# Performance work log

Measured on AMD Instinct MI355X. Metric: run time of the kernel, lower is better.

Reference implementation:

```python
import jax, jax.numpy as jnp
import numpy as np

NUM_HEADS = 4

def setup_inputs() -> dict:
    key = jax.random.key(0)
    k1, k2, k3, k4 = jax.random.split(key, 4)
    B, N, D = 8, 768, 2048
    x = jax.random.normal(k1, (B, N, D), dtype=jnp.float32)
    s = 1.0 / np.sqrt(N)
    W_qk = jax.random.normal(k2, (N, N), dtype=jnp.float32) * s
    W_v = jax.random.normal(k3, (N, N), dtype=jnp.float32) * s
    W_out = jax.random.normal(k4, (N, N), dtype=jnp.float32) * s
    return {"x": x, "W_qk": W_qk, "W_v": W_v, "W_out": W_out}

def reference(x, W_qk, W_v, W_out):
    B, N, D = x.shape
    H = NUM_HEADS
    n = N // H
    y = jnp.swapaxes(x, 1, 2)                    # (B, D, N): attention over channels D
    qk = y @ W_qk.T                              # (B, D, N)
    v = y @ W_v.T                                # (B, D, N)
    # to heads: (B, D, N) -> (B, H, D, n)
    qk = jnp.swapaxes(qk.reshape(B, D, H, n), 1, 2)
    v = jnp.swapaxes(v.reshape(B, D, H, n), 1, 2)
    dot = jnp.einsum('bhdn,bhen->bhde', qk, qk)  # (B, H, D, D)
    q2 = jnp.sum(qk * qk, axis=-1)               # (B, H, D)
    # negative squared Euclidean distance logits: 2*q.k - ||q||^2 - ||k||^2
    logits = 2.0 * dot - q2[..., :, None] - q2[..., None, :]
    attn = jax.nn.softmax(logits, axis=-1)
    w = jnp.einsum('bhde,bhen->bhdn', attn, v)   # (B, H, D, n)
    # from heads: (B, H, D, n) -> (B, D, N)
    w = jnp.swapaxes(w, 1, 2).reshape(B, D, N)
    out = w @ W_out.T                            # (B, D, N)
    return jnp.swapaxes(out, 1, 2)               # (B, N, D)
```

## Files before the change

### kernel.cpp

```cpp
#include <hip/hip_runtime.h>
#include <stdint.h>

#define B_  8
#define N_  768
#define D_  2048
#define H_  4
#define HN  192

#define QROW 200
#define VROW 72
#define KTILE_B 25600
#define VTILE_B 27648

typedef unsigned short u16;
typedef float    f32x4 __attribute__((ext_vector_type(4)));
typedef __bf16   bf16x8 __attribute__((ext_vector_type(8)));
typedef uint32_t u32x4 __attribute__((ext_vector_type(4)));
typedef uint32_t u32x2 __attribute__((ext_vector_type(2)));

__device__ __forceinline__ u16 f2bf(float f) {
  uint32_t u = __builtin_bit_cast(uint32_t, f);
  u += 0x7fffu + ((u >> 16) & 1u);
  return (u16)(u >> 16);
}

typedef const __attribute__((address_space(1))) void* gas_ptr;
typedef __attribute__((address_space(3))) void* las_ptr;
__device__ __forceinline__ void gld16(const void* g, void* l) {
  __builtin_amdgcn_global_load_lds((gas_ptr)g, (las_ptr)l, 16, 0, 0);
}

__global__ __launch_bounds__(256) void transpose_x(const float* __restrict__ x,
                                                   u16* __restrict__ xt) {
  __shared__ float tile[64][65];
  const int d0 = blockIdx.x * 64;
  const int n0 = blockIdx.y * 64;
  const int b  = blockIdx.z;
  const int t   = threadIdx.x;
  const int col = t & 63;
  const int rb  = (t >> 6) * 16;
  const float* src = x + ((size_t)b * N_ + n0) * D_ + d0;
  #pragma unroll
  for (int i = 0; i < 16; i++)
    tile[rb + i][col] = src[(size_t)(rb + i) * D_ + col];
  __syncthreads();
  u16* dst = xt + ((size_t)b * D_ + d0) * N_ + n0;
  #pragma unroll
  for (int i = 0; i < 16; i++)
    dst[(size_t)(rb + i) * N_ + col] = f2bf(tile[col][rb + i]);
}

__global__ __launch_bounds__(256) void cvt_w(const float* __restrict__ a,
                                             const float* __restrict__ b,
                                             const float* __restrict__ c,
                                             u16* __restrict__ oa,
                                             u16* __restrict__ ob,
                                             u16* __restrict__ oc) {
  const float* src = (blockIdx.y == 0) ? a : ((blockIdx.y == 1) ? b : c);
  u16*         dst = (blockIdx.y == 0) ? oa : ((blockIdx.y == 1) ? ob : oc);
  const int i = (blockIdx.x * 256 + threadIdx.x) * 4;
  f32x4 v = *(const f32x4*)(src + i);
  u16 tmp[4];
  #pragma unroll
  for (int j = 0; j < 4; j++) tmp[j] = f2bf(v[j]);
  *(u32x2*)(dst + i) = *(u32x2*)tmp;
}

__global__ __launch_bounds__(256) void zero_q2(float* __restrict__ q2) {
  q2[blockIdx.x * 256 + threadIdx.x] = 0.f;
}

__global__ __launch_bounds__(256) void qkv_gemm(const u16* __restrict__ xt,
                                                const u16* __restrict__ wqk,
                                                const u16* __restrict__ wv,
                                                u16* __restrict__ qkb,
                                                u16* __restrict__ vtb,
                                                float* __restrict__ q2) {
  const int b  = blockIdx.z;
  const int dtile = blockIdx.x;
  const int d0 = dtile * 64;
  const int j0 = blockIdx.y * 64;
  const int h   = j0 / HN;
  const int jn0 = j0 - h * HN;
  const int tid  = threadIdx.x;
  const int wave = tid >> 6, lane = tid & 63;
  const int l15  = lane & 15, quad = lane >> 4;
  const int wm = wave >> 1, wn = wave & 1;

  __shared__ u16 At[64][40];
  __shared__ u16 Bq[64][40];
  __shared__ u16 Bv[64][40];
  __shared__ float ttile[64][76];

  const f32x4 fz = {0.f, 0.f, 0.f, 0.f};
  f32x4 accq[2][2], accv[2][2];
  #pragma unroll
  for (int i = 0; i < 2; i++)
    #pragma unroll
    for (int j = 0; j < 2; j++) { accq[i][j] = fz; accv[i][j] = fz; }

  const int srow = tid >> 2;
  const int soff = (tid & 3) * 8;
  const u16* ax = xt  + ((size_t)b * D_ + d0 + srow) * N_ + soff;
  const u16* bq = wqk + (size_t)(j0 + srow) * N_ + soff;
  const u16* bv = wv  + (size_t)(j0 + srow) * N_ + soff;

  for (int k0 = 0; k0 < N_; k0 += 32) {
    __syncthreads();
    *(u32x4*)&At[srow][soff] = *(const u32x4*)(ax + k0);
    *(u32x4*)&Bq[srow][soff] = *(const u32x4*)(bq + k0);
    *(u32x4*)&Bv[srow][soff] = *(const u32x4*)(bv + k0);
    __syncthreads();
    bf16x8 Af[2], Bqf[2], Bvf[2];
    #pragma unroll
    for (int mi = 0; mi < 2; mi++)
      Af[mi] = *(const bf16x8*)&At[wm * 32 + mi * 16 + l15][quad * 8];
    #pragma unroll
    for (int ni = 0; ni < 2; ni++) {
      Bqf[ni] = *(const bf16x8*)&Bq[wn * 32 + ni * 16 + l15][quad * 8];
      Bvf[ni] = *(const bf16x8*)&Bv[wn * 32 + ni * 16 + l15][quad * 8];
    }
    #pragma unroll
    for (int mi = 0; mi < 2; mi++)
      #pragma unroll
      for (int ni = 0; ni < 2; ni++) {
        accq[mi][ni] = __builtin_amdgcn_mfma_f32_16x16x32_bf16(Af[mi], Bqf[ni], accq[mi][ni], 0, 0, 0);
        accv[mi][ni] = __builtin_amdgcn_mfma_f32_16x16x32_bf16(Af[mi], Bvf[ni], accv[mi][ni], 0, 0, 0);
      }
  }

  const size_t bh = (size_t)(b * H_ + h);

  #pragma unroll
  for (int mi = 0; mi < 2; mi++)
    #pragma unroll
    for (int r = 0; r < 4; r++) {
      const int d = d0 + wm * 32 + mi * 16 + quad * 4 + r;
      float ssq = 0.f;
      #pragma unroll
      for (int ni = 0; ni < 2; ni++) {
        float val = accq[mi][ni][r];
        ssq += val * val;
      }
      ssq += __shfl_xor(ssq, 1, 64);
      ssq += __shfl_xor(ssq, 2, 64);
      ssq += __shfl_xor(ssq, 4, 64);
      ssq += __shfl_xor(ssq, 8, 64);
      if (l15 == 0) atomicAdd(&q2[bh * D_ + d], ssq);
    }

  #pragma unroll
  for (int mi = 0; mi < 2; mi++)
    #pragma unroll
    for (int ni = 0; ni < 2; ni++)
      #pragma unroll
      for (int r = 0; r < 4; r++)
        ttile[wm * 32 + mi * 16 + quad * 4 + r][wn * 32 + ni * 16 + l15] = accq[mi][ni][r];
  __syncthreads();
  u16* qtbase = qkb + bh * (size_t)(D_ * QROW);
  #pragma unroll
  for (int i = 0; i < 2; i++) {
    const int p = tid + i * 256;
    const int d = p & 63, g8 = p >> 6;
    u16 tmp[8];
    #pragma unroll
    for (int j = 0; j < 8; j++) tmp[j] = f2bf(ttile[d][g8 * 8 + j]);
    *(u32x4*)(qtbase + (size_t)(d0 + d) * QROW + jn0 + g8 * 8) = *(u32x4*)tmp;
  }
  __syncthreads();

  #pragma unroll
  for (int mi = 0; mi < 2; mi++)
    #pragma unroll
    for (int ni = 0; ni < 2; ni++)
      *(f32x4*)&ttile[wn * 32 + ni * 16 + l15][wm * 32 + mi * 16 + quad * 4] = accv[mi][ni];
  __syncthreads();
  u16* vtbase = vtb + bh * (size_t)(32 * HN * VROW) + (size_t)dtile * (HN * VROW);
  #pragma unroll
  for (int i = 0; i < 2; i++) {
    const int p = tid + i * 256;
    const int jn = p & 63, e8 = p >> 6;
    u16 tmp[8];
    #pragma unroll
    for (int j = 0; j < 8; j++) tmp[j] = f2bf(ttile[jn][e8 * 8 + j]);
    *(u32x4*)(vtbase + (size_t)(jn0 + jn) * VROW + e8 * 8) = *(u32x4*)tmp;
  }
}

__global__ __launch_bounds__(256, 2) void attn_kernel(const u16* __restrict__ qkb,
                                                      const u16* __restrict__ vtb,
                                                      const float* __restrict__ q2,
                                                      u16* __restrict__ wbuf) {
  const int bid  = blockIdx.x;
  const int bh   = (bid & 7) * 4 + (bid >> 7);
  const int dblk = (bid >> 3) & 15;
  const int b = bh >> 2, h = bh & 3;
  const int tid  = threadIdx.x;
  const int wave = tid >> 6, lane = tid & 63;
  const int l15  = lane & 15, quad = lane >> 4;

  __shared__ u16 Klds[64 * QROW];
  __shared__ u16 Vlds[HN * VROW];
  __shared__ u16 Plds[4][32][VROW];
  __shared__ float rsl[4][32];

  const u16* kg = qkb + (size_t)bh * (D_ * QROW);
  const u16* vg = vtb + (size_t)bh * (32 * HN * VROW);
  const float* q2g = q2 + (size_t)bh * D_;

  bf16x8 Qf[2][6];
  {
    const u16* qrow = kg + (size_t)(dblk * 128 + wave * 32 + l15) * QROW + quad * 8;
    #pragma unroll
    for (int nt = 0; nt < 2; nt++)
      #pragma unroll
      for (int f = 0; f < 6; f++)
        Qf[nt][f] = *(const bf16x8*)(qrow + (size_t)nt * 16 * QROW + f * 32);
  }
  float cd[2];
  cd[0] = q2g[dblk * 128 + wave * 32 + l15];
  cd[1] = q2g[dblk * 128 + wave * 32 + 16 + l15];

  const f32x4 fz = {0.f, 0.f, 0.f, 0.f};
  f32x4 O[2][12];
  #pragma unroll
  for (int mt = 0; mt < 2; mt++)
    #pragma unroll
    for (int c = 0; c < 12; c++) O[mt][c] = fz;
  float rsp[2] = {0.f, 0.f};

  for (int t = 0; t < 32; t++) {
    __syncthreads();
    {
      const char* ks = (const char*)kg + (size_t)t * KTILE_B;
      char* kd = (char*)Klds;
      for (int c = wave; c < 25; c += 4)
        gld16(ks + c * 1024 + lane * 16, kd + c * 1024 + lane * 16);
      const char* vs = (const char*)vg + (size_t)t * VTILE_B;
      char* vd = (char*)Vlds;
      for (int c = wave; c < 27; c += 4)
        gld16(vs + c * 1024 + lane * 16, vd + c * 1024 + lane * 16);
    }
    __syncthreads();

    #pragma unroll
    for (int et = 0; et < 4; et++) {
      bf16x8 Kf[6];
      #pragma unroll
      for (int f = 0; f < 6; f++)
        Kf[f] = *(const bf16x8*)&Klds[(et * 16 + l15) * QROW + f * 32 + quad * 8];
      f32x4 S0 = fz, S1 = fz;
      #pragma unroll
      for (int f = 0; f < 6; f++) {
        S0 = __builtin_amdgcn_mfma_f32_16x16x32_bf16(Kf[f], Qf[0][f], S0, 0, 0, 0);
        S1 = __builtin_amdgcn_mfma_f32_16x16x32_bf16(Kf[f], Qf[1][f], S1, 0, 0, 0);
      }
      const f32x4 ce = *(const f32x4*)&q2g[t * 64 + et * 16 + quad * 4];
      u16 pk0[4], pk1[4];
      #pragma unroll
      for (int r = 0; r < 4; r++) {
        float p0 = __expf(__builtin_fmaf(S0[r], 2.f, -(ce[r] + cd[0])));
        float p1 = __expf(__builtin_fmaf(S1[r], 2.f, -(ce[r] + cd[1])));
        rsp[0] += p0; rsp[1] += p1;
        pk0[r] = f2bf(p0); pk1[r] = f2bf(p1);
      }
      *(u32x2*)&Plds[wave][l15][et * 16 + quad * 4]      = *(u32x2*)pk0;
      *(u32x2*)&Plds[wave][16 + l15][et * 16 + quad * 4] = *(u32x2*)pk1;
    }

    #pragma unroll
    for (int kk = 0; kk < 2; kk++) {
      bf16x8 Pf0 = *(const bf16x8*)&Plds[wave][l15][kk * 32 + quad * 8];
      bf16x8 Pf1 = *(const bf16x8*)&Plds[wave][16 + l15][kk * 32 + quad * 8];
      #pragma unroll
      for (int c = 0; c < 12; c++) {
        bf16x8 Vf = *(const bf16x8*)&Vlds[(c * 16 + l15) * VROW + kk * 32 + quad * 8];
        O[0][c] = __builtin_amdgcn_mfma_f32_16x16x32_bf16(Pf0, Vf, O[0][c], 0, 0, 0);
        O[1][c] = __builtin_amdgcn_mfma_f32_16x16x32_bf16(Pf1, Vf, O[1][c], 0, 0, 0);
      }
    }
  }

  #pragma unroll
  for (int nt = 0; nt < 2; nt++) {
    float s = rsp[nt];
    s += __shfl_xor(s, 16, 64);
    s += __shfl_xor(s, 32, 64);
    if (quad == 0) rsl[wave][nt * 16 + l15] = s;
  }
  __builtin_amdgcn_s_waitcnt(0);
  #pragma unroll
  for (int mt = 0; mt < 2; mt++)
    #pragma unroll
    for (int r = 0; r < 4; r++) {
      const float inv = 1.f / rsl[wave][mt * 16 + quad * 4 + r];
      const int d = dblk * 128 + wave * 32 + mt * 16 + quad * 4 + r;
      u16* wrow = wbuf + ((size_t)b * D_ + d) * N_ + h * HN;
      #pragma unroll
      for (int c = 0; c < 12; c++)
        wrow[c * 16 + l15] = f2bf(O[mt][c][r] * inv);
    }
}

__global__ __launch_bounds__(256) void out_gemm(const u16* __restrict__ wbuf,
                                                const u16* __restrict__ wout,
                                                float* __restrict__ outp) {
  const int b  = blockIdx.z;
  const int d0 = blockIdx.x * 64;
  const int i0 = blockIdx.y * 64;
  const int tid  = threadIdx.x;
  const int wave = tid >> 6, lane = tid & 63;
  const int l15  = lane & 15, quad = lane >> 4;
  const int wm = wave >> 1, wn = wave & 1;

  __shared__ u16 At[64][40];
  __shared__ u16 Bt[64][40];
  __shared__ float otile[64][68];

  const f32x4 fz = {0.f, 0.f, 0.f, 0.f};
  f32x4 acc[2][2];
  #pragma unroll
  for (int i = 0; i < 2; i++)
    #pragma unroll
    for (int j = 0; j < 2; j++) acc[i][j] = fz;

  const int srow = tid >> 2;
  const int soff = (tid & 3) * 8;
  const u16* ax = wbuf + ((size_t)b * D_ + d0 + srow) * N_ + soff;
  const u16* bw = wout + (size_t)(i0 + srow) * N_ + soff;

  for (int k0 = 0; k0 < N_; k0 += 32) {
    __syncthreads();
    *(u32x4*)&At[srow][soff] = *(const u32x4*)(ax + k0);
    *(u32x4*)&Bt[srow][soff] = *(const u32x4*)(bw + k0);
    __syncthreads();
    bf16x8 Af[2], Bf[2];
    #pragma unroll
    for (int mi = 0; mi < 2; mi++)
      Af[mi] = *(const bf16x8*)&At[wm * 32 + mi * 16 + l15][quad * 8];
    #pragma unroll
    for (int ni = 0; ni < 2; ni++)
      Bf[ni] = *(const bf16x8*)&Bt[wn * 32 + ni * 16 + l15][quad * 8];
    #pragma unroll
    for (int mi = 0; mi < 2; mi++)
      #pragma unroll
      for (int ni = 0; ni < 2; ni++)
        acc[mi][ni] = __builtin_amdgcn_mfma_f32_16x16x32_bf16(Af[mi], Bf[ni], acc[mi][ni], 0, 0, 0);
  }

  #pragma unroll
  for (int mi = 0; mi < 2; mi++)
    #pragma unroll
    for (int ni = 0; ni < 2; ni++)
      #pragma unroll
      for (int r = 0; r < 4; r++)
        otile[wn * 32 + ni * 16 + l15][wm * 32 + mi * 16 + quad * 4 + r] = acc[mi][ni][r];
  __syncthreads();
  const int il = tid >> 2;
  const int ch = (tid & 3) * 16;
  float* orow = outp + ((size_t)b * N_ + i0 + il) * D_ + d0 + ch;
  #pragma unroll
  for (int i = 0; i < 16; i += 4)
    *(f32x4*)(orow + i) = *(const f32x4*)&otile[il][ch + i];
}

extern "C" void kernel_launch(void* const* d_in, const int* in_sizes, int n_in,
                              void* d_out, int out_size, void* d_ws, size_t ws_size,
                              hipStream_t stream) {
  (void)in_sizes; (void)n_in; (void)out_size; (void)ws_size;
  const float* x    = (const float*)d_in[0];
  const float* Wqk  = (const float*)d_in[1];
  const float* Wv   = (const float*)d_in[2];
  const float* Wout = (const float*)d_in[3];
  float* outp = (float*)d_out;

  char* ws = (char*)d_ws;
  size_t off = 0;
  u16* xt   = (u16*)(ws + off); off += (size_t)B_ * D_ * N_ * 2;
  u16* qkb  = (u16*)(ws + off); off += (size_t)B_ * H_ * D_ * QROW * 2;
  u16* vtb  = (u16*)(ws + off); off += (size_t)B_ * H_ * 32 * HN * VROW * 2;
  float* q2 = (float*)(ws + off); off += (size_t)B_ * H_ * D_ * 4;
  u16* wqk_bf  = (u16*)(ws + off); off += (size_t)N_ * N_ * 2;
  u16* wv_bf   = (u16*)(ws + off); off += (size_t)N_ * N_ * 2;
  u16* wout_bf = (u16*)(ws + off); off += (size_t)N_ * N_ * 2;
  u16* wbuf = xt;

  transpose_x<<<dim3(D_ / 64, N_ / 64, B_), 256, 0, stream>>>(x, xt);
  cvt_w<<<dim3((N_ * N_) / (256 * 4), 3), 256, 0, stream>>>(Wqk, Wv, Wout, wqk_bf, wv_bf, wout_bf);
  zero_q2<<<dim3((B_ * H_ * D_) / 256), 256, 0, stream>>>(q2);
  qkv_gemm<<<dim3(D_ / 64, N_ / 64, B_), 256, 0, stream>>>(xt, wqk_bf, wv_bf, qkb, vtb, q2);
  attn_kernel<<<dim3((D_ / 128) * B_ * H_), 256, 0, stream>>>(qkb, vtb, q2, wbuf);
  out_gemm<<<dim3(D_ / 64, N_ / 64, B_), 256, 0, stream>>>(wbuf, wout_bf, outp);
}
```

Measured before the change: 350.0 us.

## Enlarge QKV and output GEMM tiles to 128x128 with direct-to-LDS loads

Both projection GEMMs move from 64x64 to 128x128 block tiles with a 4x4 MFMA fragment per wave, which raises reuse of the LDS-staged operands. Global tiles are staged with gld16 direct global-to-LDS copies instead of register round-trips. For the Q tile the MFMA operands are swapped to produce a transposed accumulator, so both epilogues write bf16 straight from registers and the LDS transpose tiles and their barriers are dropped. The costs are more accumulator registers (launch bound set to 2 blocks per SIMD), fewer blocks in flight, and less coalesced 8-byte epilogue stores.

```diff
diff --git a/kernel.cpp b/kernel.cpp
--- a/kernel.cpp
+++ b/kernel.cpp
@@ -70,120 +70,110 @@
   q2[blockIdx.x * 256 + threadIdx.x] = 0.f;
 }
 
-__global__ __launch_bounds__(256) void qkv_gemm(const u16* __restrict__ xt,
-                                                const u16* __restrict__ wqk,
-                                                const u16* __restrict__ wv,
-                                                u16* __restrict__ qkb,
-                                                u16* __restrict__ vtb,
-                                                float* __restrict__ q2) {
-  const int b  = blockIdx.z;
+__global__ __launch_bounds__(256, 2) void qkv_gemm(const u16* __restrict__ xt,
+                                                   const u16* __restrict__ wqk,
+                                                   const u16* __restrict__ wv,
+                                                   u16* __restrict__ qkb,
+                                                   u16* __restrict__ vtb,
+                                                   float* __restrict__ q2) {
+  const int b     = blockIdx.z;
   const int dtile = blockIdx.x;
-  const int d0 = dtile * 64;
-  const int j0 = blockIdx.y * 64;
-  const int h   = j0 / HN;
-  const int jn0 = j0 - h * HN;
+  const int d0    = dtile * 128;
+  const int j0    = blockIdx.y * 128;
   const int tid  = threadIdx.x;
   const int wave = tid >> 6, lane = tid & 63;
   const int l15  = lane & 15, quad = lane >> 4;
   const int wm = wave >> 1, wn = wave & 1;
 
-  __shared__ u16 At[64][40];
-  __shared__ u16 Bq[64][40];
-  __shared__ u16 Bv[64][40];
-  __shared__ float ttile[64][76];
+  __shared__ u16 At[128 * 32];
+  __shared__ u16 Bq[128 * 32];
+  __shared__ u16 Bv[128 * 32];
 
   const f32x4 fz = {0.f, 0.f, 0.f, 0.f};
-  f32x4 accq[2][2], accv[2][2];
-  #pragma unroll
-  for (int i = 0; i < 2; i++)
-    #pragma unroll
-    for (int j = 0; j < 2; j++) { accq[i][j] = fz; accv[i][j] = fz; }
-
-  const int srow = tid >> 2;
-  const int soff = (tid & 3) * 8;
-  const u16* ax = xt  + ((size_t)b * D_ + d0 + srow) * N_ + soff;
-  const u16* bq = wqk + (size_t)(j0 + srow) * N_ + soff;
-  const u16* bv = wv  + (size_t)(j0 + srow) * N_ + soff;
+  f32x4 accq[4][4];
+  f32x4 accv[4][4];
+  #pragma unroll
+  for (int i = 0; i < 4; i++)
+    #pragma unroll
+    for (int j = 0; j < 4; j++) { accq[i][j] = fz; accv[i][j] = fz; }
+
+  const int srow  = tid >> 2;
+  const int sbyte = (tid & 3) * 16;
+  const u16* ax = xt  + ((size_t)b * D_ + d0 + srow) * N_;
+  const u16* bq = wqk + (size_t)(j0 + srow) * N_;
+  const u16* bv = wv  + (size_t)(j0 + srow) * N_;
 
   for (int k0 = 0; k0 < N_; k0 += 32) {
     __syncthreads();
-    *(u32x4*)&At[srow][soff] = *(const u32x4*)(ax + k0);
-    *(u32x4*)&Bq[srow][soff] = *(const u32x4*)(bq + k0);
-    *(u32x4*)&Bv[srow][soff] = *(const u32x4*)(bv + k0);
-    __syncthreads();
-    bf16x8 Af[2], Bqf[2], Bvf[2];
-    #pragma unroll
-    for (int mi = 0; mi < 2; mi++)
-      Af[mi] = *(const bf16x8*)&At[wm * 32 + mi * 16 + l15][quad * 8];
-    #pragma unroll
-    for (int ni = 0; ni < 2; ni++) {
-      Bqf[ni] = *(const bf16x8*)&Bq[wn * 32 + ni * 16 + l15][quad * 8];
-      Bvf[ni] = *(const bf16x8*)&Bv[wn * 32 + ni * 16 + l15][quad * 8];
-    }
-    #pragma unroll
-    for (int mi = 0; mi < 2; mi++)
-      #pragma unroll
-      for (int ni = 0; ni < 2; ni++) {
-        accq[mi][ni] = __builtin_amdgcn_mfma_f32_16x16x32_bf16(Af[mi], Bqf[ni], accq[mi][ni], 0, 0, 0);
-        accv[mi][ni] = __builtin_amdgcn_mfma_f32_16x16x32_bf16(Af[mi], Bvf[ni], accv[mi][ni], 0, 0, 0);
+    #pragma unroll
+    for (int c = 0; c < 2; c++) {
+      gld16((const char*)(ax + (size_t)c * 64 * N_ + k0) + sbyte,
+            (char*)At + c * 4096 + tid * 16);
+      gld16((const char*)(bq + (size_t)c * 64 * N_ + k0) + sbyte,
+            (char*)Bq + c * 4096 + tid * 16);
+      gld16((const char*)(bv + (size_t)c * 64 * N_ + k0) + sbyte,
+            (char*)Bv + c * 4096 + tid * 16);
+    }
+    __syncthreads();
+
+    bf16x8 Af[4];
+    #pragma unroll
+    for (int mi = 0; mi < 4; mi++)
+      Af[mi] = *(const bf16x8*)&At[(wm * 64 + mi * 16 + l15) * 32 + quad * 8];
+    #pragma unroll
+    for (int ni = 0; ni < 4; ni++) {
+      bf16x8 Bqf = *(const bf16x8*)&Bq[(wn * 64 + ni * 16 + l15) * 32 + quad * 8];
+      bf16x8 Bvf = *(const bf16x8*)&Bv[(wn * 64 + ni * 16 + l15) * 32 + quad * 8];
+      #pragma unroll
+      for (int mi = 0; mi < 4; mi++) {
+        accq[ni][mi] = __builtin_amdgcn_mfma_f32_16x16x32_bf16(Bqf, Af[mi], accq[ni][mi], 0, 0, 0);
+        accv[mi][ni] = __builtin_amdgcn_mfma_f32_16x16x32_bf16(Af[mi], Bvf, accv[mi][ni], 0, 0, 0);
       }
-  }
-
-  const size_t bh = (size_t)(b * H_ + h);
-
-  #pragma unroll
-  for (int mi = 0; mi < 2; mi++)
-    #pragma unroll
-    for (int r = 0; r < 4; r++) {
-      const int d = d0 + wm * 32 + mi * 16 + quad * 4 + r;
-      float ssq = 0.f;
-      #pragma unroll
-      for (int ni = 0; ni < 2; ni++) {
-        float val = accq[mi][ni][r];
-        ssq += val * val;
-      }
-      ssq += __shfl_xor(ssq, 1, 64);
-      ssq += __shfl_xor(ssq, 2, 64);
-      ssq += __shfl_xor(ssq, 4, 64);
-      ssq += __shfl_xor(ssq, 8, 64);
-      if (l15 == 0) atomicAdd(&q2[bh * D_ + d], ssq);
-    }
-
-  #pragma unroll
-  for (int mi = 0; mi < 2; mi++)
-    #pragma unroll
-    for (int ni = 0; ni < 2; ni++)
-      #pragma unroll
-      for (int r = 0; r < 4; r++)
-        ttile[wm * 32 + mi * 16 + quad * 4 + r][wn * 32 + ni * 16 + l15] = accq[mi][ni][r];
-  __syncthreads();
+    }
+  }
+
+  const int h_w  = (j0 + wn * 64) / HN;
+  const int jn_w = (j0 + wn * 64) % HN;
+  const size_t bh = (size_t)b * H_ + h_w;
+
+  #pragma unroll
+  for (int md = 0; md < 4; md++) {
+    float s = 0.f;
+    #pragma unroll
+    for (int nj = 0; nj < 4; nj++)
+      #pragma unroll
+      for (int r = 0; r < 4; r++) { float v = accq[nj][md][r]; s += v * v; }
+    s += __shfl_xor(s, 16, 64);
+    s += __shfl_xor(s, 32, 64);
+    if (quad == 0)
+      atomicAdd(&q2[bh * D_ + d0 + wm * 64 + md * 16 + l15], s);
+  }
+
   u16* qtbase = qkb + bh * (size_t)(D_ * QROW);
   #pragma unroll
-  for (int i = 0; i < 2; i++) {
-    const int p = tid + i * 256;
-    const int d = p & 63, g8 = p >> 6;
-    u16 tmp[8];
-    #pragma unroll
-    for (int j = 0; j < 8; j++) tmp[j] = f2bf(ttile[d][g8 * 8 + j]);
-    *(u32x4*)(qtbase + (size_t)(d0 + d) * QROW + jn0 + g8 * 8) = *(u32x4*)tmp;
-  }
-  __syncthreads();
-
-  #pragma unroll
-  for (int mi = 0; mi < 2; mi++)
-    #pragma unroll
-    for (int ni = 0; ni < 2; ni++)
-      *(f32x4*)&ttile[wn * 32 + ni * 16 + l15][wm * 32 + mi * 16 + quad * 4] = accv[mi][ni];
-  __syncthreads();
-  u16* vtbase = vtb + bh * (size_t)(32 * HN * VROW) + (size_t)dtile * (HN * VROW);
-  #pragma unroll
-  for (int i = 0; i < 2; i++) {
-    const int p = tid + i * 256;
-    const int jn = p & 63, e8 = p >> 6;
-    u16 tmp[8];
-    #pragma unroll
-    for (int j = 0; j < 8; j++) tmp[j] = f2bf(ttile[jn][e8 * 8 + j]);
-    *(u32x4*)(vtbase + (size_t)(jn0 + jn) * VROW + e8 * 8) = *(u32x4*)tmp;
+  for (int md = 0; md < 4; md++) {
+    const size_t dro = (size_t)(d0 + wm * 64 + md * 16 + l15) * QROW;
+    #pragma unroll
+    for (int nj = 0; nj < 4; nj++) {
+      u16 tmp[4];
+      #pragma unroll
+      for (int r = 0; r < 4; r++) tmp[r] = f2bf(accq[nj][md][r]);
+      *(u32x2*)(qtbase + dro + jn_w + nj * 16 + quad * 4) = *(u32x2*)tmp;
+    }
+  }
+
+  const int etile = dtile * 2 + wm;
+  u16* vtbase = vtb + bh * (size_t)(32 * HN * VROW) + (size_t)etile * (HN * VROW);
+  #pragma unroll
+  for (int ni = 0; ni < 4; ni++) {
+    const size_t jro = (size_t)(jn_w + ni * 16 + l15) * VROW;
+    #pragma unroll
+    for (int mi = 0; mi < 4; mi++) {
+      u16 tmp[4];
+      #pragma unroll
+      for (int r = 0; r < 4; r++) tmp[r] = f2bf(accv[mi][ni][r]);
+      *(u32x2*)(vtbase + jro + mi * 16 + quad * 4) = *(u32x2*)tmp;
+    }
   }
 }
 
@@ -302,66 +292,64 @@
     }
 }
 
-__global__ __launch_bounds__(256) void out_gemm(const u16* __restrict__ wbuf,
-                                                const u16* __restrict__ wout,
-                                                float* __restrict__ outp) {
+__global__ __launch_bounds__(256, 2) void out_gemm(const u16* __restrict__ wbuf,
+                                                   const u16* __restrict__ wout,
+                                                   float* __restrict__ outp) {
   const int b  = blockIdx.z;
-  const int d0 = blockIdx.x * 64;
-  const int i0 = blockIdx.y * 64;
+  const int d0 = blockIdx.x * 128;
+  const int i0 = blockIdx.y * 128;
   const int tid  = threadIdx.x;
   const int wave = tid >> 6, lane = tid & 63;
   const int l15  = lane & 15, quad = lane >> 4;
   const int wm = wave >> 1, wn = wave & 1;
 
-  __shared__ u16 At[64][40];
-  __shared__ u16 Bt[64][40];
-  __shared__ float otile[64][68];
+  __shared__ u16 At[128 * 32];
+  __shared__ u16 Bt[128 * 32];
 
   const f32x4 fz = {0.f, 0.f, 0.f, 0.f};
-  f32x4 acc[2][2];
-  #pragma unroll
-  for (int i = 0; i < 2; i++)
-    #pragma unroll
-    for (int j = 0; j < 2; j++) acc[i][j] = fz;
-
-  const int srow = tid >> 2;
-  const int soff = (tid & 3) * 8;
-  const u16* ax = wbuf + ((size_t)b * D_ + d0 + srow) * N_ + soff;
-  const u16* bw = wout + (size_t)(i0 + srow) * N_ + soff;
+  f32x4 acc[4][4];
+  #pragma unroll
+  for (int i = 0; i < 4; i++)
+    #pragma unroll
+    for (int j = 0; j < 4; j++) acc[i][j] = fz;
+
+  const int srow  = tid >> 2;
+  const int sbyte = (tid & 3) * 16;
+  const u16* ax = wbuf + ((size_t)b * D_ + d0 + srow) * N_;
+  const u16* bw = wout + (size_t)(i0 + srow) * N_;
 
   for (int k0 = 0; k0 < N_; k0 += 32) {
     __syncthreads();
-    *(u32x4*)&At[srow][soff] = *(const u32x4*)(ax + k0);
-    *(u32x4*)&Bt[srow][soff] = *(const u32x4*)(bw + k0);
-    __syncthreads();
-    bf16x8 Af[2], Bf[2];
-    #pragma unroll
-    for (int mi = 0; mi < 2; mi++)
-      Af[mi] = *(const bf16x8*)&At[wm * 32 + mi * 16 + l15][quad * 8];
-    #pragma unroll
-    for (int ni = 0; ni < 2; ni++)
-      Bf[ni] = *(const bf16x8*)&Bt[wn * 32 + ni * 16 + l15][quad * 8];
-    #pragma unroll
-    for (int mi = 0; mi < 2; mi++)
-      #pragma unroll
-      for (int ni = 0; ni < 2; ni++)
-        acc[mi][ni] = __builtin_amdgcn_mfma_f32_16x16x32_bf16(Af[mi], Bf[ni], acc[mi][ni], 0, 0, 0);
-  }
-
-  #pragma unroll
-  for (int mi = 0; mi < 2; mi++)
-    #pragma unroll
-    for (int ni = 0; ni < 2; ni++)
-      #pragma unroll
-      for (int r = 0; r < 4; r++)
-        otile[wn * 32 + ni * 16 + l15][wm * 32 + mi * 16 + quad * 4 + r] = acc[mi][ni][r];
-  __syncthreads();
-  const int il = tid >> 2;
-  const int ch = (tid & 3) * 16;
-  float* orow = outp + ((size_t)b * N_ + i0 + il) * D_ + d0 + ch;
-  #pragma unroll
-  for (int i = 0; i < 16; i += 4)
-    *(f32x4*)(orow + i) = *(const f32x4*)&otile[il][ch + i];
+    #pragma unroll
+    for (int c = 0; c < 2; c++) {
+      gld16((const char*)(ax + (size_t)c * 64 * N_ + k0) + sbyte,
+            (char*)At + c * 4096 + tid * 16);
+      gld16((const char*)(bw + (size_t)c * 64 * N_ + k0) + sbyte,
+            (char*)Bt + c * 4096 + tid * 16);
+    }
+    __syncthreads();
+
+    bf16x8 Af[4];
+    #pragma unroll
+    for (int mi = 0; mi < 4; mi++)
+      Af[mi] = *(const bf16x8*)&At[(wm * 64 + mi * 16 + l15) * 32 + quad * 8];
+    #pragma unroll
+    for (int ni = 0; ni < 4; ni++) {
+      bf16x8 Bf = *(const bf16x8*)&Bt[(wn * 64 + ni * 16 + l15) * 32 + quad * 8];
+      #pragma unroll
+      for (int mi = 0; mi < 4; mi++)
+        acc[mi][ni] = __builtin_amdgcn_mfma_f32_16x16x32_bf16(Af[mi], Bf, acc[mi][ni], 0, 0, 0);
+    }
+  }
+
+  #pragma unroll
+  for (int ni = 0; ni < 4; ni++) {
+    float* orow = outp + ((size_t)b * N_ + i0 + wn * 64 + ni * 16 + l15) * D_
+                + d0 + wm * 64 + quad * 4;
+    #pragma unroll
+    for (int mi = 0; mi < 4; mi++)
+      *(f32x4*)(orow + mi * 16) = acc[mi][ni];
+  }
 }
 
 extern "C" void kernel_launch(void* const* d_in, const int* in_sizes, int n_in,
@@ -388,7 +376,7 @@
   transpose_x<<<dim3(D_ / 64, N_ / 64, B_), 256, 0, stream>>>(x, xt);
   cvt_w<<<dim3((N_ * N_) / (256 * 4), 3), 256, 0, stream>>>(Wqk, Wv, Wout, wqk_bf, wv_bf, wout_bf);
   zero_q2<<<dim3((B_ * H_ * D_) / 256), 256, 0, stream>>>(q2);
-  qkv_gemm<<<dim3(D_ / 64, N_ / 64, B_), 256, 0, stream>>>(xt, wqk_bf, wv_bf, qkb, vtb, q2);
+  qkv_gemm<<<dim3(D_ / 128, N_ / 128, B_), 256, 0, stream>>>(xt, wqk_bf, wv_bf, qkb, vtb, q2);
   attn_kernel<<<dim3((D_ / 128) * B_ * H_), 256, 0, stream>>>(qkb, vtb, q2, wbuf);
-  out_gemm<<<dim3(D_ / 64, N_ / 64, B_), 256, 0, stream>>>(wbuf, wout_bf, outp);
-}
+  out_gemm<<<dim3(D_ / 128, N_ / 128, B_), 256, 0, stream>>>(wbuf, wout_bf, outp);
+}
```

Result: faster. 303.8 us (-13.2%).
